# Optimization experiments

Hardware: AMD Instinct MI355X
Metric: run time of the kernel (lower is better)

The kernel has to match this reference:

```python
import jax, jax.numpy as jnp
import numpy as np

NUM_CLASSES = 21
NUM_BOXES = 8732
BATCH = 128


def setup_inputs() -> dict:
    key = jax.random.key(0)
    k1, k2, k3, k4 = jax.random.split(key, 4)
    return {
        "loc_preds": jax.random.normal(k1, (BATCH, NUM_BOXES, 4), dtype=jnp.float32),
        "loc_targets": jax.random.normal(k2, (BATCH, NUM_BOXES, 4), dtype=jnp.float32),
        "conf_preds": jax.random.normal(k3, (BATCH, NUM_BOXES, NUM_CLASSES), dtype=jnp.float32),
        "label_targets": jax.random.randint(k4, (BATCH, NUM_BOXES), 0, NUM_CLASSES, dtype=jnp.int64),
    }


def reference(loc_preds, loc_targets, conf_preds, label_targets):
    n, num_boxes, _ = conf_preds.shape
    pos = label_targets > 0                                   # [n, B] matched boxes
    num_matched = jnp.sum(pos).astype(conf_preds.dtype)

    # --- localization loss: smooth L1 (beta=1) summed over positive boxes ---
    diff = loc_preds - loc_targets
    ad = jnp.abs(diff)
    sl1 = jnp.where(ad < 1.0, 0.5 * diff * diff, ad - 0.5)    # [n, B, 4]
    loc_loss = jnp.sum(jnp.where(pos[:, :, None], sl1, 0.0))

    # --- per-box CE for mining (original uses a single global max for logsumexp) ---
    x_max = jax.lax.stop_gradient(jnp.max(conf_preds))
    lse = jnp.log(jnp.sum(jnp.exp(conf_preds - x_max), axis=-1)) + x_max   # [n, B]
    gold = jnp.take_along_axis(conf_preds, label_targets[..., None], axis=-1)[..., 0]
    mining_loss = jnp.where(pos, -1.0, lse - gold)            # pos boxes forced lowest

    # --- hard negative mining: double argsort -> rank of each box's loss ---
    idx = jnp.argsort(-mining_loss, axis=1)                   # descending sort indices
    rank = jnp.argsort(idx, axis=1)                           # rank of each box
    num_pos = jnp.sum(pos.astype(jnp.int32), axis=1)          # [n]
    num_neg = jnp.minimum(3 * num_pos, num_boxes - 1)         # [n]
    neg = rank < num_neg[:, None]
    sel = pos | neg                                           # [n, B]

    # --- confidence loss: standard CE over selected boxes (F.cross_entropy) ---
    logp = jax.nn.log_softmax(conf_preds, axis=-1)
    ce = -jnp.take_along_axis(logp, label_targets[..., None], axis=-1)[..., 0]
    conf_loss = jnp.sum(jnp.where(sel, ce, 0.0))

    denom = jnp.maximum(num_matched, 1.0)
    return (loc_loss + conf_loss) / denom
```

## Files before the change

kernel.cpp:

```cpp
#include <hip/hip_runtime.h>

#define NB 8732
#define NC 21
#define BATCH 128

__device__ inline float wred_f(float v) {
#pragma unroll
    for (int o = 32; o > 0; o >>= 1) v += __shfl_down(v, o, 64);
    return v;
}
__device__ inline int wred_i(int v) {
#pragma unroll
    for (int o = 32; o > 0; o >>= 1) v += __shfl_down(v, o, 64);
    return v;
}

__global__ void __launch_bounds__(256)
kA(const float* __restrict__ locp, const float* __restrict__ loct,
   const float* __restrict__ conf, const int* __restrict__ lab,
   float* __restrict__ row_ce, float* __restrict__ row_pce,
   int* __restrict__ row_np, float* __restrict__ loc_acc) {
    const int r = blockIdx.y;
    const int i = blockIdx.x * 256 + threadIdx.x;
    float ce = 0.f, pce = 0.f, ll = 0.f;
    int pc = 0;
    if (i < NB) {
        const long box = (long)r * NB + i;
        const int l = lab[box];
        const float* cp = conf + box * (long)NC;
        float c[NC];
#pragma unroll
        for (int j = 0; j < NC; j++) c[j] = cp[j];
        float m = c[0];
#pragma unroll
        for (int j = 1; j < NC; j++) m = fmaxf(m, c[j]);
        float s = 0.f;
#pragma unroll
        for (int j = 0; j < NC; j++) s += __expf(c[j] - m);
        const float lse = m + __logf(s);
        const float gold = cp[l];
        ce = lse - gold;
        const bool pos = l > 0;

        const float4 lp = *(const float4*)(locp + box * 4);
        const float4 lt = *(const float4*)(loct + box * 4);
        float sl = 0.f, d, ad;
        d = lp.x - lt.x; ad = fabsf(d); sl += (ad < 1.f) ? 0.5f * d * d : ad - 0.5f;
        d = lp.y - lt.y; ad = fabsf(d); sl += (ad < 1.f) ? 0.5f * d * d : ad - 0.5f;
        d = lp.z - lt.z; ad = fabsf(d); sl += (ad < 1.f) ? 0.5f * d * d : ad - 0.5f;
        d = lp.w - lt.w; ad = fabsf(d); sl += (ad < 1.f) ? 0.5f * d * d : ad - 0.5f;
        if (pos) { pc = 1; pce = ce; ll = sl; }
    }

    __shared__ float sr[3][4];
    __shared__ int si[4];
    float v0 = wred_f(ce), v1 = wred_f(pce), v2 = wred_f(ll);
    int v3 = wred_i(pc);
    const int w = threadIdx.x >> 6, ln = threadIdx.x & 63;
    if (ln == 0) { sr[0][w] = v0; sr[1][w] = v1; sr[2][w] = v2; si[w] = v3; }
    __syncthreads();
    if (threadIdx.x == 0) {
        float A = 0, B = 0, C = 0; int D = 0;
#pragma unroll
        for (int k = 0; k < 4; k++) { A += sr[0][k]; B += sr[1][k]; C += sr[2][k]; D += si[k]; }
        atomicAdd(&row_ce[r], A);
        atomicAdd(&row_pce[r], B);
        atomicAdd(loc_acc, C);
        atomicAdd(&row_np[r], D);
    }
}

__device__ inline float ce_for_box(const float* __restrict__ cp) {
    float c[NC];
#pragma unroll
    for (int j = 0; j < NC; j++) c[j] = cp[j];
    float m = c[0];
#pragma unroll
    for (int j = 1; j < NC; j++) m = fmaxf(m, c[j]);
    float s = 0.f;
#pragma unroll
    for (int j = 0; j < NC; j++) s += __expf(c[j] - m);
    return m + __logf(s) - c[0];
}

__global__ void __launch_bounds__(256)
kB(const float* __restrict__ conf, const int* __restrict__ lab,
   const float* __restrict__ row_ce, const float* __restrict__ row_pce,
   const int* __restrict__ row_np, float* __restrict__ conf_acc) {
    const int r = blockIdx.x;
    const int np = row_np[r];
    const int K = min(3 * np, NB - 1);
    const int nneg = NB - np;

    if (K >= nneg) {
        if (threadIdx.x == 0) atomicAdd(conf_acc, row_ce[r]);
        return;
    }
    if (K <= 0) {
        if (threadIdx.x == 0) atomicAdd(conf_acc, row_pce[r]);
        return;
    }

    __shared__ unsigned key[NB];
    __shared__ unsigned hist[256];
    __shared__ unsigned sb[2];

    for (int i = threadIdx.x; i < NB; i += 256) {
        const long box = (long)r * NB + i;
        unsigned k = 0u;
        if (lab[box] == 0) {
            float ce = ce_for_box(conf + box * (long)NC);
            k = __float_as_uint(fmaxf(ce, 0.f));
        }
        key[i] = k;
    }
    __syncthreads();

    unsigned prefix = 0;
    int Kr = K;
    for (int round = 3; round >= 0; --round) {
        const int sh = round * 8;
        const unsigned pmask = (round == 3) ? 0u : (0xFFFFFFFFu << (8 * (round + 1)));
        for (int b = threadIdx.x; b < 256; b += 256) hist[b] = 0;
        __syncthreads();
        for (int i = threadIdx.x; i < NB; i += 256) {
            const unsigned k = key[i];
            if ((k & pmask) == prefix) atomicAdd(&hist[(k >> sh) & 255u], 1u);
        }
        __syncthreads();
        if (threadIdx.x == 0) {
            unsigned cum = 0; int b = 255;
            for (; b > 0; --b) {
                const unsigned h = hist[b];
                if (cum + h >= (unsigned)Kr) break;
                cum += h;
            }
            sb[0] = cum; sb[1] = (unsigned)b;
        }
        __syncthreads();
        const unsigned cum = sb[0];
        const int b = (int)sb[1];
        Kr -= (int)cum;
        prefix |= ((unsigned)b << sh);
        __syncthreads();
    }

    float local = 0.f;
    for (int i = threadIdx.x; i < NB; i += 256) {
        const unsigned k = key[i];
        if (k > prefix) local += __uint_as_float(k);
    }
    __shared__ float sred[4];
    float v = wred_f(local);
    const int w = threadIdx.x >> 6, ln = threadIdx.x & 63;
    if (ln == 0) sred[w] = v;
    __syncthreads();
    if (threadIdx.x == 0) {
        float tot = sred[0] + sred[1] + sred[2] + sred[3];
        tot += (float)Kr * __uint_as_float(prefix);
        atomicAdd(conf_acc, row_pce[r] + tot);
    }
}

__global__ void kC(const float* __restrict__ loc_acc, const float* __restrict__ conf_acc,
                   const int* __restrict__ row_np, float* __restrict__ out) {
    if (threadIdx.x == 0 && blockIdx.x == 0) {
        int nm = 0;
        for (int r = 0; r < BATCH; r++) nm += row_np[r];
        const float denom = fmaxf((float)nm, 1.f);
        out[0] = (loc_acc[0] + conf_acc[0]) / denom;
    }
}

extern "C" void kernel_launch(void* const* d_in, const int* in_sizes, int n_in,
                              void* d_out, int out_size, void* d_ws, size_t ws_size,
                              hipStream_t stream) {
    const float* locp = (const float*)d_in[0];
    const float* loct = (const float*)d_in[1];
    const float* conf = (const float*)d_in[2];
    const int* lab = (const int*)d_in[3];
    float* out = (float*)d_out;

    float* loc_acc = (float*)d_ws;
    float* conf_acc = loc_acc + 1;
    float* row_ce = (float*)d_ws + 16;
    float* row_pce = row_ce + BATCH;
    int* row_np = (int*)(row_pce + BATCH);

    hipMemsetAsync(d_ws, 0, 4096, stream);

    dim3 gA((NB + 255) / 256, BATCH);
    hipLaunchKernelGGL(kA, gA, dim3(256), 0, stream,
                       locp, loct, conf, lab, row_ce, row_pce, row_np, loc_acc);
    hipLaunchKernelGGL(kB, dim3(BATCH), dim3(256), 0, stream,
                       conf, lab, row_ce, row_pce, row_np, conf_acc);
    hipLaunchKernelGGL(kC, dim3(1), dim3(1), 0, stream,
                       loc_acc, conf_acc, row_np, out);
}
```

Measured before the change: 200.3 us.

## Stage conf tile through shared memory with coalesced loads and fuse final kernel

kA now loads each block's contiguous conf slice into LDS with aligned float4 loads, then each thread reads its 21 logits from LDS instead of strided global reads. The gold logit comes from registers. The final reduction kernel is removed: kB uses a done counter and the last block writes the output, with num-matched tracked by an extra atomic. This reduces uncoalesced global traffic and one launch, at the cost of about 21KB of LDS per block, which lowers occupancy.

```diff
diff --git a/kernel.cpp b/kernel.cpp
--- a/kernel.cpp
+++ b/kernel.cpp
@@ -3,6 +3,8 @@
 #define NB 8732
 #define NC 21
 #define BATCH 128
+#define TILE 256
+#define CBUF 5384
 
 __device__ inline float wred_f(float v) {
 #pragma unroll
@@ -19,27 +21,43 @@
 kA(const float* __restrict__ locp, const float* __restrict__ loct,
    const float* __restrict__ conf, const int* __restrict__ lab,
    float* __restrict__ row_ce, float* __restrict__ row_pce,
-   int* __restrict__ row_np, float* __restrict__ loc_acc) {
+   int* __restrict__ row_np, float* __restrict__ loc_acc,
+   int* __restrict__ nm_acc) {
+    __shared__ float cb[CBUF];
     const int r = blockIdx.y;
-    const int i = blockIdx.x * 256 + threadIdx.x;
+    const int b0 = blockIdx.x * TILE;
+    const int cnt = min(TILE, NB - b0);
+
+    const size_t o0 = ((size_t)r * NB + b0) * NC;
+    const size_t a0 = o0 & ~(size_t)3;
+    const int shift = (int)(o0 - a0);
+    const int ndw = shift + cnt * NC;
+    const int nvec = (ndw + 3) >> 2;
+    const float4* src = (const float4*)(conf + a0);
+    for (int v = threadIdx.x; v < nvec; v += 256) {
+        float4 x = src[v];
+        cb[4 * v + 0] = x.x; cb[4 * v + 1] = x.y;
+        cb[4 * v + 2] = x.z; cb[4 * v + 3] = x.w;
+    }
+    __syncthreads();
+
     float ce = 0.f, pce = 0.f, ll = 0.f;
     int pc = 0;
-    if (i < NB) {
-        const long box = (long)r * NB + i;
-        const int l = lab[box];
-        const float* cp = conf + box * (long)NC;
+    const int t = threadIdx.x;
+    if (t < cnt) {
+        const int base = shift + t * NC;
         float c[NC];
 #pragma unroll
-        for (int j = 0; j < NC; j++) c[j] = cp[j];
+        for (int j = 0; j < NC; j++) c[j] = cb[base + j];
         float m = c[0];
 #pragma unroll
         for (int j = 1; j < NC; j++) m = fmaxf(m, c[j]);
         float s = 0.f;
 #pragma unroll
         for (int j = 0; j < NC; j++) s += __expf(c[j] - m);
-        const float lse = m + __logf(s);
-        const float gold = cp[l];
-        ce = lse - gold;
+        const long box = (long)r * NB + b0 + t;
+        const int l = lab[box];
+        ce = m + __logf(s) - c[l];
         const bool pos = l > 0;
 
         const float4 lp = *(const float4*)(locp + box * 4);
@@ -67,10 +85,11 @@
         atomicAdd(&row_pce[r], B);
         atomicAdd(loc_acc, C);
         atomicAdd(&row_np[r], D);
-    }
-}
-
-__device__ inline float ce_for_box(const float* __restrict__ cp) {
+        atomicAdd(nm_acc, D);
+    }
+}
+
+__device__ inline float ce_for_box0(const float* __restrict__ cp) {
     float c[NC];
 #pragma unroll
     for (int j = 0; j < NC; j++) c[j] = cp[j];
@@ -86,89 +105,83 @@
 __global__ void __launch_bounds__(256)
 kB(const float* __restrict__ conf, const int* __restrict__ lab,
    const float* __restrict__ row_ce, const float* __restrict__ row_pce,
-   const int* __restrict__ row_np, float* __restrict__ conf_acc) {
+   const int* __restrict__ row_np, float* __restrict__ conf_acc,
+   float* __restrict__ loc_acc, int* __restrict__ nm_acc,
+   int* __restrict__ done, float* __restrict__ out) {
     const int r = blockIdx.x;
     const int np = row_np[r];
     const int K = min(3 * np, NB - 1);
     const int nneg = NB - np;
 
+    float rowval = 0.f;
     if (K >= nneg) {
-        if (threadIdx.x == 0) atomicAdd(conf_acc, row_ce[r]);
-        return;
-    }
-    if (K <= 0) {
-        if (threadIdx.x == 0) atomicAdd(conf_acc, row_pce[r]);
-        return;
-    }
-
-    __shared__ unsigned key[NB];
-    __shared__ unsigned hist[256];
-    __shared__ unsigned sb[2];
-
-    for (int i = threadIdx.x; i < NB; i += 256) {
-        const long box = (long)r * NB + i;
-        unsigned k = 0u;
-        if (lab[box] == 0) {
-            float ce = ce_for_box(conf + box * (long)NC);
-            k = __float_as_uint(fmaxf(ce, 0.f));
-        }
-        key[i] = k;
-    }
-    __syncthreads();
-
-    unsigned prefix = 0;
-    int Kr = K;
-    for (int round = 3; round >= 0; --round) {
-        const int sh = round * 8;
-        const unsigned pmask = (round == 3) ? 0u : (0xFFFFFFFFu << (8 * (round + 1)));
-        for (int b = threadIdx.x; b < 256; b += 256) hist[b] = 0;
+        rowval = row_ce[r];
+    } else if (K <= 0) {
+        rowval = row_pce[r];
+    } else {
+        __shared__ unsigned key[NB];
+        __shared__ unsigned hist[256];
+        __shared__ unsigned sb[2];
+        for (int i = threadIdx.x; i < NB; i += 256) {
+            const long box = (long)r * NB + i;
+            unsigned k = 0u;
+            if (lab[box] == 0) {
+                float ce = ce_for_box0(conf + box * (long)NC);
+                k = __float_as_uint(fmaxf(ce, 0.f));
+            }
+            key[i] = k;
+        }
         __syncthreads();
+        unsigned prefix = 0;
+        int Kr = K;
+        for (int round = 3; round >= 0; --round) {
+            const int sh = round * 8;
+            const unsigned pmask = (round == 3) ? 0u : (0xFFFFFFFFu << (8 * (round + 1)));
+            for (int b = threadIdx.x; b < 256; b += 256) hist[b] = 0;
+            __syncthreads();
+            for (int i = threadIdx.x; i < NB; i += 256) {
+                const unsigned k = key[i];
+                if ((k & pmask) == prefix) atomicAdd(&hist[(k >> sh) & 255u], 1u);
+            }
+            __syncthreads();
+            if (threadIdx.x == 0) {
+                unsigned cum = 0; int b = 255;
+                for (; b > 0; --b) {
+                    const unsigned h = hist[b];
+                    if (cum + h >= (unsigned)Kr) break;
+                    cum += h;
+                }
+                sb[0] = cum; sb[1] = (unsigned)b;
+            }
+            __syncthreads();
+            Kr -= (int)sb[0];
+            prefix |= (sb[1] << sh);
+            __syncthreads();
+        }
+        float local = 0.f;
         for (int i = threadIdx.x; i < NB; i += 256) {
             const unsigned k = key[i];
-            if ((k & pmask) == prefix) atomicAdd(&hist[(k >> sh) & 255u], 1u);
-        }
+            if (k > prefix) local += __uint_as_float(k);
+        }
+        __shared__ float sred[4];
+        float v = wred_f(local);
+        const int w = threadIdx.x >> 6, ln = threadIdx.x & 63;
+        if (ln == 0) sred[w] = v;
         __syncthreads();
-        if (threadIdx.x == 0) {
-            unsigned cum = 0; int b = 255;
-            for (; b > 0; --b) {
-                const unsigned h = hist[b];
-                if (cum + h >= (unsigned)Kr) break;
-                cum += h;
-            }
-            sb[0] = cum; sb[1] = (unsigned)b;
-        }
-        __syncthreads();
-        const unsigned cum = sb[0];
-        const int b = (int)sb[1];
-        Kr -= (int)cum;
-        prefix |= ((unsigned)b << sh);
-        __syncthreads();
-    }
-
-    float local = 0.f;
-    for (int i = threadIdx.x; i < NB; i += 256) {
-        const unsigned k = key[i];
-        if (k > prefix) local += __uint_as_float(k);
-    }
-    __shared__ float sred[4];
-    float v = wred_f(local);
-    const int w = threadIdx.x >> 6, ln = threadIdx.x & 63;
-    if (ln == 0) sred[w] = v;
-    __syncthreads();
+        rowval = row_pce[r] + sred[0] + sred[1] + sred[2] + sred[3]
+               + (float)Kr * __uint_as_float(prefix);
+    }
+
     if (threadIdx.x == 0) {
-        float tot = sred[0] + sred[1] + sred[2] + sred[3];
-        tot += (float)Kr * __uint_as_float(prefix);
-        atomicAdd(conf_acc, row_pce[r] + tot);
-    }
-}
-
-__global__ void kC(const float* __restrict__ loc_acc, const float* __restrict__ conf_acc,
-                   const int* __restrict__ row_np, float* __restrict__ out) {
-    if (threadIdx.x == 0 && blockIdx.x == 0) {
-        int nm = 0;
-        for (int r = 0; r < BATCH; r++) nm += row_np[r];
-        const float denom = fmaxf((float)nm, 1.f);
-        out[0] = (loc_acc[0] + conf_acc[0]) / denom;
+        atomicAdd(conf_acc, rowval);
+        __threadfence();
+        const int old = atomicAdd(done, 1);
+        if (old == BATCH - 1) {
+            const float cf = atomicAdd(conf_acc, 0.f);
+            const float lc = atomicAdd(loc_acc, 0.f);
+            const int nm = atomicAdd(nm_acc, 0);
+            out[0] = (lc + cf) / fmaxf((float)nm, 1.f);
+        }
     }
 }
 
@@ -183,17 +196,17 @@
 
     float* loc_acc = (float*)d_ws;
     float* conf_acc = loc_acc + 1;
+    int* nm_acc = (int*)d_ws + 2;
+    int* done = (int*)d_ws + 3;
     float* row_ce = (float*)d_ws + 16;
     float* row_pce = row_ce + BATCH;
     int* row_np = (int*)(row_pce + BATCH);
 
     hipMemsetAsync(d_ws, 0, 4096, stream);
 
-    dim3 gA((NB + 255) / 256, BATCH);
+    dim3 gA((NB + TILE - 1) / TILE, BATCH);
     hipLaunchKernelGGL(kA, gA, dim3(256), 0, stream,
-                       locp, loct, conf, lab, row_ce, row_pce, row_np, loc_acc);
+                       locp, loct, conf, lab, row_ce, row_pce, row_np, loc_acc, nm_acc);
     hipLaunchKernelGGL(kB, dim3(BATCH), dim3(256), 0, stream,
-                       conf, lab, row_ce, row_pce, row_np, conf_acc);
-    hipLaunchKernelGGL(kC, dim3(1), dim3(1), 0, stream,
-                       loc_acc, conf_acc, row_np, out);
-}
+                       conf, lab, row_ce, row_pce, row_np, conf_acc, loc_acc, nm_acc, done, out);
+}
```

New measurement: 256.1 us. +27.8%, slower.

## Fuse final reduction into kB via last-block pattern, load loc only for positives

Applied to the files above, without the earlier changes.

Removes the single-thread kC launch by having the last kB block to finish, detected with an atomic counter, perform the final reduction. Per-row accumulators are padded to 16 floats to spread the atomics. kA now reads loc predictions and targets only for positive boxes, and picks the gold logit from registers instead of a second global load. This trades one kernel launch and some global traffic for threadfence and atomic-counter overhead plus branch divergence on the loc loads.

```diff
diff --git a/kernel.cpp b/kernel.cpp
--- a/kernel.cpp
+++ b/kernel.cpp
@@ -3,6 +3,7 @@
 #define NB 8732
 #define NC 21
 #define BATCH 128
+#define BX 35
 
 __device__ inline float wred_f(float v) {
 #pragma unroll
@@ -14,20 +15,24 @@
     for (int o = 32; o > 0; o >>= 1) v += __shfl_down(v, o, 64);
     return v;
 }
+
+#define WS_DONE 0
+#define WS_KBOUT 16
+#define WS_ROWACC 256
+#define WS_ZERO_BYTES 12288
 
 __global__ void __launch_bounds__(256)
 kA(const float* __restrict__ locp, const float* __restrict__ loct,
    const float* __restrict__ conf, const int* __restrict__ lab,
-   float* __restrict__ row_ce, float* __restrict__ row_pce,
-   int* __restrict__ row_np, float* __restrict__ loc_acc) {
+   float* __restrict__ ws) {
     const int r = blockIdx.y;
     const int i = blockIdx.x * 256 + threadIdx.x;
     float ce = 0.f, pce = 0.f, ll = 0.f;
     int pc = 0;
     if (i < NB) {
-        const long box = (long)r * NB + i;
+        const size_t box = (size_t)r * NB + i;
         const int l = lab[box];
-        const float* cp = conf + box * (long)NC;
+        const float* cp = conf + box * (size_t)NC;
         float c[NC];
 #pragma unroll
         for (int j = 0; j < NC; j++) c[j] = cp[j];
@@ -37,19 +42,20 @@
         float s = 0.f;
 #pragma unroll
         for (int j = 0; j < NC; j++) s += __expf(c[j] - m);
-        const float lse = m + __logf(s);
-        const float gold = cp[l];
-        ce = lse - gold;
-        const bool pos = l > 0;
-
-        const float4 lp = *(const float4*)(locp + box * 4);
-        const float4 lt = *(const float4*)(loct + box * 4);
-        float sl = 0.f, d, ad;
-        d = lp.x - lt.x; ad = fabsf(d); sl += (ad < 1.f) ? 0.5f * d * d : ad - 0.5f;
-        d = lp.y - lt.y; ad = fabsf(d); sl += (ad < 1.f) ? 0.5f * d * d : ad - 0.5f;
-        d = lp.z - lt.z; ad = fabsf(d); sl += (ad < 1.f) ? 0.5f * d * d : ad - 0.5f;
-        d = lp.w - lt.w; ad = fabsf(d); sl += (ad < 1.f) ? 0.5f * d * d : ad - 0.5f;
-        if (pos) { pc = 1; pce = ce; ll = sl; }
+        float gold = c[0];
+#pragma unroll
+        for (int j = 1; j < NC; j++) gold = (j == l) ? c[j] : gold;
+        ce = m + __logf(s) - gold;
+        if (l > 0) {
+            pc = 1; pce = ce;
+            const float4 lp = *(const float4*)(locp + box * 4);
+            const float4 lt = *(const float4*)(loct + box * 4);
+            float d, ad;
+            d = lp.x - lt.x; ad = fabsf(d); ll += (ad < 1.f) ? 0.5f * d * d : ad - 0.5f;
+            d = lp.y - lt.y; ad = fabsf(d); ll += (ad < 1.f) ? 0.5f * d * d : ad - 0.5f;
+            d = lp.z - lt.z; ad = fabsf(d); ll += (ad < 1.f) ? 0.5f * d * d : ad - 0.5f;
+            d = lp.w - lt.w; ad = fabsf(d); ll += (ad < 1.f) ? 0.5f * d * d : ad - 0.5f;
+        }
     }
 
     __shared__ float sr[3][4];
@@ -63,14 +69,15 @@
         float A = 0, B = 0, C = 0; int D = 0;
 #pragma unroll
         for (int k = 0; k < 4; k++) { A += sr[0][k]; B += sr[1][k]; C += sr[2][k]; D += si[k]; }
-        atomicAdd(&row_ce[r], A);
-        atomicAdd(&row_pce[r], B);
-        atomicAdd(loc_acc, C);
-        atomicAdd(&row_np[r], D);
-    }
-}
-
-__device__ inline float ce_for_box(const float* __restrict__ cp) {
+        float* acc = ws + WS_ROWACC + r * 16;
+        atomicAdd(&acc[0], A);
+        atomicAdd(&acc[1], B);
+        atomicAdd(&acc[2], C);
+        atomicAdd((int*)&acc[3], D);
+    }
+}
+
+__device__ inline float ce_for_box0(const float* __restrict__ cp) {
     float c[NC];
 #pragma unroll
     for (int j = 0; j < NC; j++) c[j] = cp[j];
@@ -85,90 +92,106 @@
 
 __global__ void __launch_bounds__(256)
 kB(const float* __restrict__ conf, const int* __restrict__ lab,
-   const float* __restrict__ row_ce, const float* __restrict__ row_pce,
-   const int* __restrict__ row_np, float* __restrict__ conf_acc) {
+   float* __restrict__ ws, float* __restrict__ out) {
     const int r = blockIdx.x;
-    const int np = row_np[r];
+    const float* acc = ws + WS_ROWACC + r * 16;
+    const int np = __float_as_int(__int_as_float(((const int*)acc)[3]));
     const int K = min(3 * np, NB - 1);
     const int nneg = NB - np;
-
+    const float row_ce = acc[0];
+    const float row_pce = acc[1];
+
+    float rowval = 0.f;
     if (K >= nneg) {
-        if (threadIdx.x == 0) atomicAdd(conf_acc, row_ce[r]);
-        return;
-    }
-    if (K <= 0) {
-        if (threadIdx.x == 0) atomicAdd(conf_acc, row_pce[r]);
-        return;
-    }
-
-    __shared__ unsigned key[NB];
-    __shared__ unsigned hist[256];
-    __shared__ unsigned sb[2];
-
-    for (int i = threadIdx.x; i < NB; i += 256) {
-        const long box = (long)r * NB + i;
-        unsigned k = 0u;
-        if (lab[box] == 0) {
-            float ce = ce_for_box(conf + box * (long)NC);
-            k = __float_as_uint(fmaxf(ce, 0.f));
-        }
-        key[i] = k;
-    }
-    __syncthreads();
-
-    unsigned prefix = 0;
-    int Kr = K;
-    for (int round = 3; round >= 0; --round) {
-        const int sh = round * 8;
-        const unsigned pmask = (round == 3) ? 0u : (0xFFFFFFFFu << (8 * (round + 1)));
-        for (int b = threadIdx.x; b < 256; b += 256) hist[b] = 0;
+        rowval = row_ce;
+    } else if (K <= 0) {
+        rowval = row_pce;
+    } else {
+        __shared__ unsigned key[NB];
+        __shared__ unsigned hist[256];
+        __shared__ unsigned sb[2];
+        for (int i = threadIdx.x; i < NB; i += 256) {
+            const size_t box = (size_t)r * NB + i;
+            unsigned k = 0u;
+            if (lab[box] == 0) {
+                float ce = ce_for_box0(conf + box * (size_t)NC);
+                k = __float_as_uint(fmaxf(ce, 0.f));
+            }
+            key[i] = k;
+        }
         __syncthreads();
+        unsigned prefix = 0;
+        int Kr = K;
+        for (int round = 3; round >= 0; --round) {
+            const int sh = round * 8;
+            const unsigned pmask = (round == 3) ? 0u : (0xFFFFFFFFu << (8 * (round + 1)));
+            for (int b = threadIdx.x; b < 256; b += 256) hist[b] = 0;
+            __syncthreads();
+            for (int i = threadIdx.x; i < NB; i += 256) {
+                const unsigned k = key[i];
+                if ((k & pmask) == prefix) atomicAdd(&hist[(k >> sh) & 255u], 1u);
+            }
+            __syncthreads();
+            if (threadIdx.x == 0) {
+                unsigned cum = 0; int b = 255;
+                for (; b > 0; --b) {
+                    const unsigned h = hist[b];
+                    if (cum + h >= (unsigned)Kr) break;
+                    cum += h;
+                }
+                sb[0] = cum; sb[1] = (unsigned)b;
+            }
+            __syncthreads();
+            Kr -= (int)sb[0];
+            prefix |= (sb[1] << sh);
+            __syncthreads();
+        }
+        float local = 0.f;
         for (int i = threadIdx.x; i < NB; i += 256) {
             const unsigned k = key[i];
-            if ((k & pmask) == prefix) atomicAdd(&hist[(k >> sh) & 255u], 1u);
-        }
+            if (k > prefix) local += __uint_as_float(k);
+        }
+        __shared__ float sred[4];
+        float v = wred_f(local);
+        const int ww = threadIdx.x >> 6, lnn = threadIdx.x & 63;
+        if (lnn == 0) sred[ww] = v;
+        __syncthreads();
+        rowval = row_pce + sred[0] + sred[1] + sred[2] + sred[3]
+               + (float)Kr * __uint_as_float(prefix);
+    }
+
+    __shared__ int islast;
+    if (threadIdx.x == 0) {
+        ws[WS_KBOUT + r] = rowval;
+        __threadfence();
+        const int old = atomicAdd((int*)ws + WS_DONE, 1);
+        islast = (old == BATCH - 1) ? 1 : 0;
+    }
+    __syncthreads();
+    if (islast) {
+        __threadfence();
+        float cf = 0.f, lc = 0.f;
+        int nm = 0;
+        if (threadIdx.x < BATCH) {
+            const int t = threadIdx.x;
+            cf = ws[WS_KBOUT + t];
+            const float* a = ws + WS_ROWACC + t * 16;
+            lc = a[2];
+            nm = ((const int*)a)[3];
+        }
+        __shared__ float sf[4], sl[4];
+        __shared__ int sn[4];
+        float vc = wred_f(cf), vl = wred_f(lc);
+        int vn = wred_i(nm);
+        const int w = threadIdx.x >> 6, ln = threadIdx.x & 63;
+        if (ln == 0) { sf[w] = vc; sl[w] = vl; sn[w] = vn; }
         __syncthreads();
         if (threadIdx.x == 0) {
-            unsigned cum = 0; int b = 255;
-            for (; b > 0; --b) {
-                const unsigned h = hist[b];
-                if (cum + h >= (unsigned)Kr) break;
-                cum += h;
-            }
-            sb[0] = cum; sb[1] = (unsigned)b;
-        }
-        __syncthreads();
-        const unsigned cum = sb[0];
-        const int b = (int)sb[1];
-        Kr -= (int)cum;
-        prefix |= ((unsigned)b << sh);
-        __syncthreads();
-    }
-
-    float local = 0.f;
-    for (int i = threadIdx.x; i < NB; i += 256) {
-        const unsigned k = key[i];
-        if (k > prefix) local += __uint_as_float(k);
-    }
-    __shared__ float sred[4];
-    float v = wred_f(local);
-    const int w = threadIdx.x >> 6, ln = threadIdx.x & 63;
-    if (ln == 0) sred[w] = v;
-    __syncthreads();
-    if (threadIdx.x == 0) {
-        float tot = sred[0] + sred[1] + sred[2] + sred[3];
-        tot += (float)Kr * __uint_as_float(prefix);
-        atomicAdd(conf_acc, row_pce[r] + tot);
-    }
-}
-
-__global__ void kC(const float* __restrict__ loc_acc, const float* __restrict__ conf_acc,
-                   const int* __restrict__ row_np, float* __restrict__ out) {
-    if (threadIdx.x == 0 && blockIdx.x == 0) {
-        int nm = 0;
-        for (int r = 0; r < BATCH; r++) nm += row_np[r];
-        const float denom = fmaxf((float)nm, 1.f);
-        out[0] = (loc_acc[0] + conf_acc[0]) / denom;
+            float CF = sf[0] + sf[1] + sf[2] + sf[3];
+            float LC = sl[0] + sl[1] + sl[2] + sl[3];
+            int NM = sn[0] + sn[1] + sn[2] + sn[3];
+            out[0] = (LC + CF) / fmaxf((float)NM, 1.f);
+        }
     }
 }
 
@@ -180,20 +203,12 @@
     const float* conf = (const float*)d_in[2];
     const int* lab = (const int*)d_in[3];
     float* out = (float*)d_out;
-
-    float* loc_acc = (float*)d_ws;
-    float* conf_acc = loc_acc + 1;
-    float* row_ce = (float*)d_ws + 16;
-    float* row_pce = row_ce + BATCH;
-    int* row_np = (int*)(row_pce + BATCH);
-
-    hipMemsetAsync(d_ws, 0, 4096, stream);
-
-    dim3 gA((NB + 255) / 256, BATCH);
-    hipLaunchKernelGGL(kA, gA, dim3(256), 0, stream,
-                       locp, loct, conf, lab, row_ce, row_pce, row_np, loc_acc);
+    float* ws = (float*)d_ws;
+
+    hipMemsetAsync(d_ws, 0, WS_ZERO_BYTES, stream);
+
+    hipLaunchKernelGGL(kA, dim3(BX, BATCH), dim3(256), 0, stream,
+                       locp, loct, conf, lab, ws);
     hipLaunchKernelGGL(kB, dim3(BATCH), dim3(256), 0, stream,
-                       conf, lab, row_ce, row_pce, row_np, conf_acc);
-    hipLaunchKernelGGL(kC, dim3(1), dim3(1), 0, stream,
-                       loc_acc, conf_acc, row_np, out);
-}
+                       conf, lab, ws, out);
+}
```

Measured after the change: 178.4 us. -10.9%, faster.
